# Performance work log

Hardware: AMD Instinct MI355X
Metric: run time of the kernel (lower is better)

Reference implementation:

```python
import jax, jax.numpy as jnp
import numpy as np
import math

B, L, C, H = 8, 1024, 1024, 8
EPS = 1e-5

def setup_inputs() -> dict:
    key = jax.random.key(0)
    ks = jax.random.split(key, 5)
    s = 0.02
    return {
        "x": jax.random.normal(ks[0], (B, L, C), dtype=jnp.float32),
        "ln_g": jnp.ones((C,), dtype=jnp.float32),
        "ln_b": jnp.zeros((C,), dtype=jnp.float32),
        "w_qkv": jax.random.normal(ks[1], (C, 3 * C), dtype=jnp.float32) * s,
        "b_qkv": jax.random.normal(ks[2], (3 * C,), dtype=jnp.float32) * s,
        "w_out": jax.random.normal(ks[3], (C, C), dtype=jnp.float32) * s,
        "b_out": jax.random.normal(ks[4], (C,), dtype=jnp.float32) * s,
    }

def reference(x, ln_g, ln_b, w_qkv, b_qkv, w_out, b_out):
    bs, length, width = x.shape
    ch = width // H
    # LayerNorm over channels
    mu = jnp.mean(x, axis=-1, keepdims=True)
    var = jnp.mean(jnp.square(x - mu), axis=-1, keepdims=True)
    xn = (x - mu) * jax.lax.rsqrt(var + EPS) * ln_g + ln_b
    # fused QKV projection
    qkv = jnp.einsum('blc,cd->bld', xn, w_qkv) + b_qkv  # [B, L, 3C]
    q, k, v = jnp.split(qkv, 3, axis=2)                 # each [B, L, C]
    scale = 1.0 / math.sqrt(math.sqrt(ch))
    # faithful raw row-major reshape as in the torch .view call
    q = (q * scale).reshape(bs * H, length, ch)
    k = (k * scale).reshape(bs * H, length, ch)
    v = v.reshape(bs * H, length, ch)
    w = jnp.einsum('bqc,bkc->bqk', q, k)                # [B*H, L, L] score matrix
    w = jax.nn.softmax(w.astype(jnp.float32), axis=-1).astype(q.dtype)
    attn = jnp.einsum('bqk,bkc->bqc', w, v).reshape(bs, length, -1)
    out = jnp.einsum('blc,cd->bld', attn, w_out) + b_out + xn  # residual uses normalized x
    return out
```

## Files before the change

kernel.cpp:

```cpp
#include <hip/hip_runtime.h>
#include <hip/hip_bf16.h>


typedef __attribute__((ext_vector_type(8))) short short8;
typedef __attribute__((ext_vector_type(4))) float f32x4;

#define QK_SCALE 0.29730177875068026f

__device__ __forceinline__ float bf2f(ushort u) {
    union { float f; unsigned int i; } c; c.i = ((unsigned int)u) << 16; return c.f;
}
__device__ __forceinline__ ushort f2bf(float f) {
    union { float f; unsigned int i; } c; c.f = f;
    unsigned int x = c.i;
    return (ushort)((x + 0x7FFFu + ((x >> 16) & 1u)) >> 16);
}

__device__ __forceinline__ void gload_lds16(const ushort* g, ushort* l) {
    __builtin_amdgcn_global_load_lds(
        (const __attribute__((address_space(1))) unsigned int*)g,
        (__attribute__((address_space(3))) unsigned int*)l, 16, 0, 0);
}

__global__ __launch_bounds__(256) void prep_kernel(
    const float* __restrict__ x, const float* __restrict__ g,
    const float* __restrict__ b, ushort* __restrict__ xn,
    const float* __restrict__ w_qkv, ushort* __restrict__ wqkvT,
    const float* __restrict__ w_out, ushort* __restrict__ woutT) {
    __shared__ ushort t[32][33];
    int bid = blockIdx.x;
    int tid = threadIdx.x;
    if (bid < 2048) {
        int w = tid >> 6, lane = tid & 63;
        int row = bid * 4 + w;
        const float* xr = x + (size_t)row * 1024;
        float v[4][4];
        float s1 = 0.f, s2 = 0.f;
#pragma unroll
        for (int j = 0; j < 4; j++) {
            float4 t4 = *(const float4*)(xr + lane * 4 + j * 256);
            v[j][0] = t4.x; v[j][1] = t4.y; v[j][2] = t4.z; v[j][3] = t4.w;
#pragma unroll
            for (int e = 0; e < 4; e++) { s1 += v[j][e]; s2 += v[j][e] * v[j][e]; }
        }
#pragma unroll
        for (int m = 32; m >= 1; m >>= 1) { s1 += __shfl_xor(s1, m); s2 += __shfl_xor(s2, m); }
        float mu = s1 * (1.0f / 1024.0f);
        float var = s2 * (1.0f / 1024.0f) - mu * mu;
        float rs = rsqrtf(var + 1e-5f);
#pragma unroll
        for (int j = 0; j < 4; j++) {
            int c0 = lane * 4 + j * 256;
            float4 gg = *(const float4*)(g + c0);
            float4 bb = *(const float4*)(b + c0);
            float gA[4] = {gg.x, gg.y, gg.z, gg.w};
            float bA[4] = {bb.x, bb.y, bb.z, bb.w};
            ushort o[4];
#pragma unroll
            for (int e = 0; e < 4; e++) o[e] = f2bf((v[j][e] - mu) * rs * gA[e] + bA[e]);
            uint2 pk;
            pk.x = (uint)o[0] | ((uint)o[1] << 16);
            pk.y = (uint)o[2] | ((uint)o[3] << 16);
            *(uint2*)(xn + (size_t)row * 1024 + c0) = pk;
        }
    } else {
        const float* in; ushort* out; int R, Cc, bx, by;
        if (bid < 5120) {
            int tt = bid - 2048;
            in = w_qkv; out = wqkvT; R = 1024; Cc = 3072;
            bx = (tt % 96) * 32; by = (tt / 96) * 32;
        } else {
            int tt = bid - 5120;
            in = w_out; out = woutT; R = 1024; Cc = 1024;
            bx = (tt % 32) * 32; by = (tt / 32) * 32;
        }
        int tx = tid & 31, ty = tid >> 5;
#pragma unroll
        for (int j = 0; j < 32; j += 8)
            t[ty + j][tx] = f2bf(in[(size_t)(by + ty + j) * Cc + bx + tx]);
        __syncthreads();
#pragma unroll
        for (int j = 0; j < 32; j += 8)
            out[(size_t)(bx + ty + j) * R + by + tx] = t[tx][ty + j];
    }
}

__global__ __launch_bounds__(256) void transpose_head(
    const ushort* __restrict__ in, ushort* __restrict__ out) {
    __shared__ ushort t[32][33];
    int h = blockIdx.z;
    int j0 = blockIdx.y * 32;
    int d0 = blockIdx.x * 32;
    int tx = threadIdx.x & 31, ty = threadIdx.x >> 5;
    const ushort* src = in + (size_t)h * 131072;
    ushort* dst = out + (size_t)h * 131072;
#pragma unroll
    for (int j = 0; j < 32; j += 8)
        t[ty + j][tx] = src[(size_t)(j0 + ty + j) * 128 + d0 + tx];
    __syncthreads();
#pragma unroll
    for (int j = 0; j < 32; j += 8)
        dst[(size_t)(d0 + ty + j) * 1024 + j0 + tx] = t[tx][ty + j];
}

__global__ __launch_bounds__(256) void gemm_qkv(
    const ushort* __restrict__ A, const ushort* __restrict__ Bt,
    const float* __restrict__ bias, ushort* __restrict__ out0,
    ushort* __restrict__ out1, ushort* __restrict__ out2) {
    const int K = 1024;
    __shared__ __align__(16) ushort As[128 * 64];
    __shared__ __align__(16) ushort Bs[128 * 64];

    int tid = threadIdx.x;
    int lane = tid & 63, w = tid >> 6;
    int l15 = lane & 15, q4 = lane >> 4;
    int wr = (w >> 1) * 64, wc = (w & 1) * 64;
    int rowBase = blockIdx.y * 128, colBase = blockIdx.x * 128;

    const ushort* aS[4]; const ushort* bS[4];
    ushort* aD[4]; ushort* bD[4];
#pragma unroll
    for (int i = 0; i < 4; i++) {
        int linear = i * 256 + w * 64 + lane;
        int r = linear >> 3;
        int l = (linear & 7) ^ (r & 7);
        aS[i] = A + (size_t)(rowBase + r) * K + l * 8;
        bS[i] = Bt + (size_t)(colBase + r) * K + l * 8;
        aD[i] = &As[linear * 8];
        bD[i] = &Bs[linear * 8];
    }

    f32x4 acc[4][4];
    f32x4 zero = {0.f, 0.f, 0.f, 0.f};
#pragma unroll
    for (int mi = 0; mi < 4; mi++)
#pragma unroll
        for (int ni = 0; ni < 4; ni++) acc[mi][ni] = zero;

    for (int kt = 0; kt < 16; kt++) {
        __syncthreads();
#pragma unroll
        for (int i = 0; i < 4; i++) {
            gload_lds16(aS[i], aD[i]);
            gload_lds16(bS[i], bD[i]);
            aS[i] += 64; bS[i] += 64;
        }
        __syncthreads();

#pragma unroll
        for (int kk = 0; kk < 2; kk++) {
            short8 aF[4], bF[4];
#pragma unroll
            for (int mi = 0; mi < 4; mi++) {
                int r = wr + mi * 16 + l15;
                aF[mi] = *(const short8*)&As[r * 64 + ((kk * 4 + q4) ^ (r & 7)) * 8];
            }
#pragma unroll
            for (int ni = 0; ni < 4; ni++) {
                int r = wc + ni * 16 + l15;
                bF[ni] = *(const short8*)&Bs[r * 64 + ((kk * 4 + q4) ^ (r & 7)) * 8];
            }
#pragma unroll
            for (int mi = 0; mi < 4; mi++)
#pragma unroll
                for (int ni = 0; ni < 4; ni++)
                    acc[mi][ni] = __builtin_amdgcn_mfma_f32_16x16x32_bf16(
                        aF[mi], bF[ni], acc[mi][ni], 0, 0, 0);
        }
    }

#pragma unroll
    for (int ni = 0; ni < 4; ni++) {
        int col = colBase + wc + ni * 16 + l15;
        float bv = bias[col];
        float sc = (col < 2048) ? QK_SCALE : 1.0f;
        int bsel = col >> 10, cc = col & 1023;
        ushort* dst = (bsel == 0) ? out0 : ((bsel == 1) ? out1 : out2);
#pragma unroll
        for (int mi = 0; mi < 4; mi++) {
            f32x4 a = acc[mi][ni];
#pragma unroll
            for (int r = 0; r < 4; r++) {
                int row = rowBase + wr + mi * 16 + q4 * 4 + r;
                dst[(size_t)row * 1024 + cc] = f2bf((a[r] + bv) * sc);
            }
        }
    }
}

__global__ __launch_bounds__(256, 4) void gemm_out(
    const ushort* __restrict__ A, const ushort* __restrict__ Bt,
    const float* __restrict__ bias, const ushort* __restrict__ resid,
    float* __restrict__ outf) {
    const int K = 1024;
    __shared__ __align__(16) ushort As[64 * 64];
    __shared__ __align__(16) ushort Bs[128 * 64];

    int tid = threadIdx.x;
    int lane = tid & 63, w = tid >> 6;
    int l15 = lane & 15, q4 = lane >> 4;
    int wr = (w >> 1) * 32, wc = (w & 1) * 64;
    int rowBase = blockIdx.y * 64, colBase = blockIdx.x * 128;

    const ushort* src[6]; ushort* dstp[6];
#pragma unroll
    for (int i = 0; i < 6; i++) {
        int id = i * 256 + w * 64 + lane;
        if (id < 512) {
            int r = id >> 3, l = (id & 7) ^ ((id >> 3) & 7);
            src[i] = A + (size_t)(rowBase + r) * K + l * 8;
            dstp[i] = &As[id * 8];
        } else {
            int idb = id - 512;
            int r = idb >> 3, l = (idb & 7) ^ ((idb >> 3) & 7);
            src[i] = Bt + (size_t)(colBase + r) * K + l * 8;
            dstp[i] = &Bs[idb * 8];
        }
    }

    f32x4 acc[2][4];
    f32x4 zero = {0.f, 0.f, 0.f, 0.f};
#pragma unroll
    for (int mi = 0; mi < 2; mi++)
#pragma unroll
        for (int ni = 0; ni < 4; ni++) acc[mi][ni] = zero;

    for (int kt = 0; kt < 16; kt++) {
        __syncthreads();
#pragma unroll
        for (int i = 0; i < 6; i++) {
            gload_lds16(src[i], dstp[i]);
            src[i] += 64;
        }
        __syncthreads();

#pragma unroll
        for (int kk = 0; kk < 2; kk++) {
            short8 aF[2], bF[4];
#pragma unroll
            for (int mi = 0; mi < 2; mi++) {
                int r = wr + mi * 16 + l15;
                aF[mi] = *(const short8*)&As[r * 64 + ((kk * 4 + q4) ^ (r & 7)) * 8];
            }
#pragma unroll
            for (int ni = 0; ni < 4; ni++) {
                int r = wc + ni * 16 + l15;
                bF[ni] = *(const short8*)&Bs[r * 64 + ((kk * 4 + q4) ^ (r & 7)) * 8];
            }
#pragma unroll
            for (int mi = 0; mi < 2; mi++)
#pragma unroll
                for (int ni = 0; ni < 4; ni++)
                    acc[mi][ni] = __builtin_amdgcn_mfma_f32_16x16x32_bf16(
                        aF[mi], bF[ni], acc[mi][ni], 0, 0, 0);
        }
    }

#pragma unroll
    for (int ni = 0; ni < 4; ni++) {
        int col = colBase + wc + ni * 16 + l15;
        float bv = bias[col];
#pragma unroll
        for (int mi = 0; mi < 2; mi++) {
            f32x4 a = acc[mi][ni];
#pragma unroll
            for (int r = 0; r < 4; r++) {
                int row = rowBase + wr + mi * 16 + q4 * 4 + r;
                outf[(size_t)row * 1024 + col] =
                    a[r] + bv + bf2f(resid[(size_t)row * 1024 + col]);
            }
        }
    }
}

__global__ __launch_bounds__(512) void attn_kernel(
    const ushort* __restrict__ qb, const ushort* __restrict__ kb,
    const ushort* __restrict__ vt, ushort* __restrict__ ob) {
    int g = blockIdx.x >> 3;
    int qblk = blockIdx.x & 7;
    const ushort* Qh = qb + (size_t)g * 131072;
    const ushort* Kh = kb + (size_t)g * 131072;
    const ushort* Vh = vt + (size_t)g * 131072;

    __shared__ __align__(16) ushort Ks[64 * 128];
    __shared__ __align__(16) ushort Vt[128 * 64];
    __shared__ __align__(16) ushort Ps[128 * 64];

    int tid = threadIdx.x, lane = tid & 63, w = tid >> 6;
    int l15 = lane & 15, q4 = lane >> 4;
    int q0 = qblk * 128;

    short8 qf[4];
#pragma unroll
    for (int ks = 0; ks < 4; ks++)
        qf[ks] = *(const short8*)&Qh[(size_t)(q0 + w * 16 + l15) * 128 + ks * 32 + q4 * 8];

    f32x4 zero = {0.f, 0.f, 0.f, 0.f};
    f32x4 o[8];
#pragma unroll
    for (int ni = 0; ni < 8; ni++) o[ni] = zero;
    float plsum[4] = {0.f, 0.f, 0.f, 0.f};

    for (int kt = 0; kt < 16; kt++) {
        __syncthreads();
#pragma unroll
        for (int i = 0; i < 2; i++) {
            int linear = i * 512 + tid;
            int r = linear >> 4, p = linear & 15;
            int l = p ^ (r & 15);
            gload_lds16(&Kh[(size_t)(kt * 64 + r) * 128 + l * 8], &Ks[linear * 8]);
        }
#pragma unroll
        for (int i = 0; i < 2; i++) {
            int linear = i * 512 + tid;
            int d = linear >> 3, p = linear & 7;
            int c = p ^ (d & 7);
            gload_lds16(&Vh[(size_t)d * 1024 + kt * 64 + c * 8], &Vt[linear * 8]);
        }
        __syncthreads();

        f32x4 sacc[4];
#pragma unroll
        for (int ni = 0; ni < 4; ni++) sacc[ni] = zero;
#pragma unroll
        for (int ks = 0; ks < 4; ks++) {
#pragma unroll
            for (int ni = 0; ni < 4; ni++) {
                int r = ni * 16 + l15;
                int p = (ks * 4 + q4) ^ (r & 15);
                short8 bF = *(const short8*)&Ks[r * 128 + p * 8];
                sacc[ni] = __builtin_amdgcn_mfma_f32_16x16x32_bf16(
                    qf[ks], bF, sacc[ni], 0, 0, 0);
            }
        }

#pragma unroll
        for (int ni = 0; ni < 4; ni++) {
#pragma unroll
            for (int r = 0; r < 4; r++) {
                float pv = __expf(sacc[ni][r]);
                plsum[r] += pv;
                int qloc = w * 16 + q4 * 4 + r;
                int key = ni * 16 + l15;
                int pc = (key >> 3) ^ (qloc & 7);
                Ps[qloc * 64 + pc * 8 + (key & 7)] = f2bf(pv);
            }
        }

#pragma unroll
        for (int ks2 = 0; ks2 < 2; ks2++) {
            int c = ks2 * 4 + q4;
            int row = w * 16 + l15;
            short8 aF = *(const short8*)&Ps[row * 64 + (c ^ (l15 & 7)) * 8];
#pragma unroll
            for (int ni = 0; ni < 8; ni++) {
                int d = ni * 16 + l15;
                short8 bF = *(const short8*)&Vt[d * 64 + (c ^ (d & 7)) * 8];
                o[ni] = __builtin_amdgcn_mfma_f32_16x16x32_bf16(aF, bF, o[ni], 0, 0, 0);
            }
        }
    }

#pragma unroll
    for (int r = 0; r < 4; r++) {
#pragma unroll
        for (int m = 1; m < 16; m <<= 1) plsum[r] += __shfl_xor(plsum[r], m, 16);
    }
    float inv[4];
#pragma unroll
    for (int r = 0; r < 4; r++) inv[r] = 1.0f / plsum[r];
#pragma unroll
    for (int ni = 0; ni < 8; ni++)
#pragma unroll
        for (int r = 0; r < 4; r++) {
            int qrow = q0 + w * 16 + q4 * 4 + r;
            ob[(size_t)g * 131072 + (size_t)qrow * 128 + ni * 16 + l15] =
                f2bf(o[ni][r] * inv[r]);
        }
}

extern "C" void kernel_launch(void* const* d_in, const int* in_sizes, int n_in,
                              void* d_out, int out_size, void* d_ws, size_t ws_size,
                              hipStream_t stream) {
    const float* x     = (const float*)d_in[0];
    const float* ln_g  = (const float*)d_in[1];
    const float* ln_b  = (const float*)d_in[2];
    const float* w_qkv = (const float*)d_in[3];
    const float* b_qkv = (const float*)d_in[4];
    const float* w_out = (const float*)d_in[5];
    const float* b_out = (const float*)d_in[6];
    float* out = (float*)d_out;

    const size_t MC = 8192ull * 1024ull;
    ushort* xn    = (ushort*)d_ws;
    ushort* wqkvT = xn + MC;
    ushort* woutT = wqkvT + 3072ull * 1024ull;
    ushort* qbuf  = woutT + 1024ull * 1024ull;
    ushort* kbuf  = qbuf + MC;
    ushort* vtbuf = kbuf + MC;
    ushort* attnb = vtbuf + MC;

    prep_kernel<<<6144, 256, 0, stream>>>(x, ln_g, ln_b, xn, w_qkv, wqkvT, w_out, woutT);
    gemm_qkv<<<dim3(24, 64), 256, 0, stream>>>(xn, wqkvT, b_qkv, qbuf, kbuf, attnb);
    transpose_head<<<dim3(4, 32, 64), 256, 0, stream>>>(attnb, vtbuf);
    attn_kernel<<<512, 512, 0, stream>>>(qbuf, kbuf, vtbuf, attnb);
    gemm_out<<<dim3(8, 128), 256, 0, stream>>>(attnb, woutT, b_out, xn, out);
}
```

Baseline: 249.5 us.

## Double-buffer QKV GEMM with 256x128 tiles, 512 threads and block swizzle

Rewrites the QKV projection GEMM to use 512-thread blocks computing 256x128 tiles. LDS is double-buffered so the next K-tile is prefetched with global_load_lds while MFMAs run, using explicit vmcnt waits and barriers plus setprio around the MFMA bursts. It also remaps the 1D grid with a swizzle to improve L2 reuse. The cost is more LDS per block (96KB), which limits occupancy, and hand-tuned wait counts that must match the number of loads issued per stage.

New measurement: 266.7 us. 1.07x slower.

```diff
diff --git a/kernel.cpp b/kernel.cpp
--- a/kernel.cpp
+++ b/kernel.cpp
@@ -103,32 +103,48 @@
         dst[(size_t)(d0 + ty + j) * 1024 + j0 + tx] = t[tx][ty + j];
 }
 
-__global__ __launch_bounds__(256) void gemm_qkv(
+__device__ __forceinline__ void stage6(const ushort* __restrict__ Ab,
+                                       const ushort* __restrict__ Bb, int t2,
+                                       ushort* AsD, ushort* BsD, int tid) {
+    const ushort* As_src = Ab + t2 * 64;
+    const ushort* Bs_src = Bb + t2 * 64;
+#pragma unroll
+    for (int i = 0; i < 4; i++) {
+        int lin = i * 512 + tid;
+        int r = lin >> 3, p = lin & 7;
+        int l = p ^ (r & 7);
+        gload_lds16(As_src + (size_t)r * 1024 + l * 8, &AsD[lin * 8]);
+    }
+#pragma unroll
+    for (int i = 0; i < 2; i++) {
+        int lin = i * 512 + tid;
+        int r = lin >> 3, p = lin & 7;
+        int l = p ^ (r & 7);
+        gload_lds16(Bs_src + (size_t)r * 1024 + l * 8, &BsD[lin * 8]);
+    }
+}
+
+__global__ __launch_bounds__(512, 2) void gemm_qkv(
     const ushort* __restrict__ A, const ushort* __restrict__ Bt,
     const float* __restrict__ bias, ushort* __restrict__ out0,
     ushort* __restrict__ out1, ushort* __restrict__ out2) {
-    const int K = 1024;
-    __shared__ __align__(16) ushort As[128 * 64];
-    __shared__ __align__(16) ushort Bs[128 * 64];
+    __shared__ __align__(16) ushort As[2][256 * 64];
+    __shared__ __align__(16) ushort Bs[2][128 * 64];
 
     int tid = threadIdx.x;
     int lane = tid & 63, w = tid >> 6;
     int l15 = lane & 15, q4 = lane >> 4;
-    int wr = (w >> 1) * 64, wc = (w & 1) * 64;
-    int rowBase = blockIdx.y * 128, colBase = blockIdx.x * 128;
-
-    const ushort* aS[4]; const ushort* bS[4];
-    ushort* aD[4]; ushort* bD[4];
-#pragma unroll
-    for (int i = 0; i < 4; i++) {
-        int linear = i * 256 + w * 64 + lane;
-        int r = linear >> 3;
-        int l = (linear & 7) ^ (r & 7);
-        aS[i] = A + (size_t)(rowBase + r) * K + l * 8;
-        bS[i] = Bt + (size_t)(colBase + r) * K + l * 8;
-        aD[i] = &As[linear * 8];
-        bD[i] = &Bs[linear * 8];
-    }
+    int wrM = (w >> 1) * 64;
+    int wcN = (w & 1) * 64;
+
+    int bid = blockIdx.x;
+    int swz = (bid & 7) * 96 + (bid >> 3);
+    int by = swz & 31;
+    int bx = swz >> 5;
+    int rowBase = by * 256, colBase = bx * 128;
+
+    const ushort* Ab = A + (size_t)rowBase * 1024;
+    const ushort* Bb = Bt + (size_t)colBase * 1024;
 
     f32x4 acc[4][4];
     f32x4 zero = {0.f, 0.f, 0.f, 0.f};
@@ -137,41 +153,63 @@
 #pragma unroll
         for (int ni = 0; ni < 4; ni++) acc[mi][ni] = zero;
 
-    for (int kt = 0; kt < 16; kt++) {
-        __syncthreads();
-#pragma unroll
-        for (int i = 0; i < 4; i++) {
-            gload_lds16(aS[i], aD[i]);
-            gload_lds16(bS[i], bD[i]);
-            aS[i] += 64; bS[i] += 64;
-        }
-        __syncthreads();
-
+    stage6(Ab, Bb, 0, &As[0][0], &Bs[0][0], tid);
+    stage6(Ab, Bb, 1, &As[1][0], &Bs[1][0], tid);
+    asm volatile("s_waitcnt vmcnt(6)" ::: "memory");
+    __builtin_amdgcn_s_barrier();
+
+    for (int t = 0; t < 16; ++t) {
+        const int cur = t & 1;
+        const ushort* Ac = &As[cur][0];
+        const ushort* Bc = &Bs[cur][0];
+
+        short8 aF[4][2], bF[4][2];
 #pragma unroll
         for (int kk = 0; kk < 2; kk++) {
-            short8 aF[4], bF[4];
 #pragma unroll
             for (int mi = 0; mi < 4; mi++) {
-                int r = wr + mi * 16 + l15;
-                aF[mi] = *(const short8*)&As[r * 64 + ((kk * 4 + q4) ^ (r & 7)) * 8];
+                int r = wrM + mi * 16 + l15;
+                aF[mi][kk] = *(const short8*)&Ac[r * 64 + ((kk * 4 + q4) ^ (r & 7)) * 8];
             }
 #pragma unroll
             for (int ni = 0; ni < 4; ni++) {
-                int r = wc + ni * 16 + l15;
-                bF[ni] = *(const short8*)&Bs[r * 64 + ((kk * 4 + q4) ^ (r & 7)) * 8];
-            }
-#pragma unroll
-            for (int mi = 0; mi < 4; mi++)
-#pragma unroll
-                for (int ni = 0; ni < 4; ni++)
-                    acc[mi][ni] = __builtin_amdgcn_mfma_f32_16x16x32_bf16(
-                        aF[mi], bF[ni], acc[mi][ni], 0, 0, 0);
+                int r = wcN + ni * 16 + l15;
+                bF[ni][kk] = *(const short8*)&Bc[r * 64 + ((kk * 4 + q4) ^ (r & 7)) * 8];
+            }
+        }
+
+        __builtin_amdgcn_s_setprio(1);
+#pragma unroll
+        for (int mi = 0; mi < 4; mi++)
+#pragma unroll
+            for (int ni = 0; ni < 4; ni++)
+                acc[mi][ni] = __builtin_amdgcn_mfma_f32_16x16x32_bf16(
+                    aF[mi][0], bF[ni][0], acc[mi][ni], 0, 0, 0);
+        __builtin_amdgcn_s_setprio(0);
+
+        asm volatile("s_waitcnt lgkmcnt(0)" ::: "memory");
+        __builtin_amdgcn_s_barrier();
+        if (t < 14) stage6(Ab, Bb, t + 2, &As[cur][0], &Bs[cur][0], tid);
+
+        __builtin_amdgcn_s_setprio(1);
+#pragma unroll
+        for (int mi = 0; mi < 4; mi++)
+#pragma unroll
+            for (int ni = 0; ni < 4; ni++)
+                acc[mi][ni] = __builtin_amdgcn_mfma_f32_16x16x32_bf16(
+                    aF[mi][1], bF[ni][1], acc[mi][ni], 0, 0, 0);
+        __builtin_amdgcn_s_setprio(0);
+
+        if (t < 15) {
+            if (t < 14) asm volatile("s_waitcnt vmcnt(6)" ::: "memory");
+            else        asm volatile("s_waitcnt vmcnt(0)" ::: "memory");
+            __builtin_amdgcn_s_barrier();
         }
     }
 
 #pragma unroll
     for (int ni = 0; ni < 4; ni++) {
-        int col = colBase + wc + ni * 16 + l15;
+        int col = colBase + wcN + ni * 16 + l15;
         float bv = bias[col];
         float sc = (col < 2048) ? QK_SCALE : 1.0f;
         int bsel = col >> 10, cc = col & 1023;
@@ -181,7 +219,7 @@
             f32x4 a = acc[mi][ni];
 #pragma unroll
             for (int r = 0; r < 4; r++) {
-                int row = rowBase + wr + mi * 16 + q4 * 4 + r;
+                int row = rowBase + wrM + mi * 16 + q4 * 4 + r;
                 dst[(size_t)row * 1024 + cc] = f2bf((a[r] + bv) * sc);
             }
         }
@@ -401,7 +439,7 @@
     ushort* attnb = vtbuf + MC;
 
     prep_kernel<<<6144, 256, 0, stream>>>(x, ln_g, ln_b, xn, w_qkv, wqkvT, w_out, woutT);
-    gemm_qkv<<<dim3(24, 64), 256, 0, stream>>>(xn, wqkvT, b_qkv, qbuf, kbuf, attnb);
+    gemm_qkv<<<768, 512, 0, stream>>>(xn, wqkvT, b_qkv, qbuf, kbuf, attnb);
     transpose_head<<<dim3(4, 32, 64), 256, 0, stream>>>(attnb, vtbuf);
     attn_kernel<<<512, 512, 0, stream>>>(qbuf, kbuf, vtbuf, attnb);
     gemm_out<<<dim3(8, 128), 256, 0, stream>>>(attnb, woutT, b_out, xn, out);
```
